# Performance work log

Measured on AMD Instinct MI355X. Metric: run time of the kernel, lower is better.

The kernel has to match this reference:

```python
import jax, jax.numpy as jnp
import numpy as np

D_MODEL = 1024
NUM_HEADS = 16
D_K = D_MODEL // NUM_HEADS


def setup_inputs() -> dict:
    key = jax.random.key(0)
    ks = jax.random.split(key, 12)
    B, S = 1, 4096
    s = 1.0 / np.sqrt(D_MODEL)
    inp = {
        'query': jax.random.normal(ks[0], (B, S, D_MODEL), jnp.float32),
        'key': jax.random.normal(ks[1], (B, S, D_MODEL), jnp.float32),
        'value': jax.random.normal(ks[2], (B, S, D_MODEL), jnp.float32),
        'W_q': jax.random.normal(ks[3], (D_MODEL, D_MODEL), jnp.float32) * s,
        'b_q': jnp.zeros((D_MODEL,), jnp.float32),
        'W_k': jax.random.normal(ks[4], (D_MODEL, D_MODEL), jnp.float32) * s,
        'b_k': jnp.zeros((D_MODEL,), jnp.float32),
        'W_v': jax.random.normal(ks[5], (D_MODEL, D_MODEL), jnp.float32) * s,
        'b_v': jnp.zeros((D_MODEL,), jnp.float32),
        'W_o': jax.random.normal(ks[6], (D_MODEL, D_MODEL), jnp.float32) * s,
        'b_o': jnp.zeros((D_MODEL,), jnp.float32),
    }
    return inp


def reference(query, key, value, W_q, b_q, W_k, b_k, W_v, b_v, W_o, b_o):
    B, S, _ = query.shape
    # torch nn.Linear: y = x @ W.T + b
    Q = query @ W_q.T + b_q
    K = key @ W_k.T + b_k
    V = value @ W_v.T + b_v
    # (B, S, H, d_k) -> (B, H, S, d_k)
    Q = Q.reshape(B, S, NUM_HEADS, D_K).transpose(0, 2, 1, 3)
    K = K.reshape(B, S, NUM_HEADS, D_K).transpose(0, 2, 1, 3)
    V = V.reshape(B, S, NUM_HEADS, D_K).transpose(0, 2, 1, 3)
    scale = 1.0 / jnp.sqrt(jnp.asarray(D_K, Q.dtype))
    qk = jnp.einsum('bhqd,bhkd->bhqk', Q, K) * scale  # [B,H,S,S]
    attn = jax.nn.softmax(qk, axis=-1)
    out = jnp.einsum('bhqk,bhkd->bhqd', attn, V)
    out = out.transpose(0, 2, 1, 3).reshape(B, S, D_MODEL)
    return out @ W_o.T + b_o
```

## Files before the change

kernel.cpp:

```cpp
#include <hip/hip_runtime.h>
#include <cstdint>
#include <cstddef>

typedef __bf16 bf16_t;
typedef _Float16 f16_t;
typedef __attribute__((ext_vector_type(8))) __bf16 bf16x8;
typedef __attribute__((ext_vector_type(4))) __bf16 bf16x4;
typedef __attribute__((ext_vector_type(2))) __bf16 bf16x2;
typedef __attribute__((ext_vector_type(8))) _Float16 f16x8;
typedef __attribute__((ext_vector_type(2))) _Float16 f16x2;
typedef __attribute__((ext_vector_type(4))) float floatx4;
typedef __attribute__((ext_vector_type(16))) float floatx16;

#define S_LEN 4096
#define DM 1024
#define NH 16
#define DKH 64
#define NSPLIT 4
#define KT_PER (S_LEN / 64 / NSPLIT)

#define QSCALE 0.1803368801111601f

__device__ __forceinline__ void async_b128(void* lds, const void* g) {
    __builtin_amdgcn_global_load_lds(
        (__attribute__((address_space(1))) void*)(uintptr_t)g,
        (__attribute__((address_space(3))) void*)lds,
        16, 0, 0);
}

__device__ __forceinline__ floatx4 mfma16(bf16x8 a, bf16x8 b, floatx4 c) {
    return __builtin_amdgcn_mfma_f32_16x16x32_bf16(a, b, c, 0, 0, 0);
}
__device__ __forceinline__ floatx16 mfma32(bf16x8 a, bf16x8 b, floatx16 c) {
    return __builtin_amdgcn_mfma_f32_32x32x16_bf16(a, b, c, 0, 0, 0);
}
__device__ __forceinline__ int f2i(float x) { return __builtin_bit_cast(int, x); }
__device__ __forceinline__ float i2f(int x) { return __builtin_bit_cast(float, x); }
__device__ __forceinline__ int p2i(bf16x2 x) { return __builtin_bit_cast(int, x); }
__device__ __forceinline__ bf16x2 i2p(int x) { return __builtin_bit_cast(bf16x2, x); }

__global__ __launch_bounds__(256) void convert_in_kernel(
    const float* __restrict__ q, const float* __restrict__ k,
    const float* __restrict__ v, bf16_t* __restrict__ dst) {
    const int z = blockIdx.z;
    const float* s = (z == 0) ? q : (z == 1) ? k : v;
    bf16_t* d = dst + (size_t)z * (S_LEN * DM);
    const size_t i = ((size_t)blockIdx.x * 256 + threadIdx.x) * 4;
    const floatx4 val = *(const floatx4*)(s + i);
    bf16x4 o;
    o[0] = (bf16_t)val[0]; o[1] = (bf16_t)val[1];
    o[2] = (bf16_t)val[2]; o[3] = (bf16_t)val[3];
    *(bf16x4*)(d + i) = o;
}

__global__ __launch_bounds__(256) void convert_w_kernel(
    const float* __restrict__ a, const float* __restrict__ b,
    const float* __restrict__ c, const float* __restrict__ e,
    bf16_t* __restrict__ dst) {
    const int z = blockIdx.z;
    const float* s = (z == 0) ? a : (z == 1) ? b : (z == 2) ? c : e;
    bf16_t* d = dst + (size_t)z * (DM * DM);
    const size_t i = ((size_t)blockIdx.x * 256 + threadIdx.x) * 4;
    const floatx4 val = *(const floatx4*)(s + i);
    bf16x4 o;
    o[0] = (bf16_t)val[0]; o[1] = (bf16_t)val[1];
    o[2] = (bf16_t)val[2]; o[3] = (bf16_t)val[3];
    *(bf16x4*)(d + i) = o;
}

template <int BN, typename OutT>
__device__ __forceinline__ void gemm_bt_body(const bf16_t* __restrict__ A,
                                             const bf16_t* __restrict__ B,
                                             const float* __restrict__ bias,
                                             OutT* __restrict__ C, float oscale) {
    constexpr int K = 1024, N = 1024;
    constexpr int NT = BN / 32;
    __shared__ bf16_t As[128 * 32];
    __shared__ bf16_t Bs[BN * 32];
    const int tid = threadIdx.x;
    const int wid = tid >> 6, lane = tid & 63;
    const int quad = lane >> 4, l16 = lane & 15;
    const int m0 = blockIdx.y * 128, n0 = blockIdx.x * BN;
    const int wm = (wid & 1) * 64, wn = (wid >> 1) * (BN / 2);

    floatx4 acc[4][NT] = {};

    for (int k0 = 0; k0 < K; k0 += 32) {
        __syncthreads();
#pragma unroll
        for (int i = 0; i < 2; ++i) {
            const int c = (i << 8) + tid;
            const int row = c >> 2;
            const int ko = (c & 3) << 3;
            const int lb = ((i << 8) + (wid << 6)) << 3;
            async_b128(&As[lb], A + (size_t)(m0 + row) * K + k0 + ko);
        }
#pragma unroll
        for (int i = 0; i < BN / 64; ++i) {
            const int c = (i << 8) + tid;
            const int row = c >> 2;
            const int ko = (c & 3) << 3;
            const int lb = ((i << 8) + (wid << 6)) << 3;
            async_b128(&Bs[lb], B + (size_t)(n0 + row) * K + k0 + ko);
        }
        __syncthreads();

        bf16x8 af[4], bfr[NT];
#pragma unroll
        for (int t = 0; t < 4; ++t)
            af[t] = *(const bf16x8*)&As[(wm + t * 16 + l16) * 32 + quad * 8];
#pragma unroll
        for (int t = 0; t < NT; ++t)
            bfr[t] = *(const bf16x8*)&Bs[(wn + t * 16 + l16) * 32 + quad * 8];
#pragma unroll
        for (int mt = 0; mt < 4; ++mt)
#pragma unroll
            for (int nt = 0; nt < NT; ++nt)
                acc[mt][nt] = mfma16(af[mt], bfr[nt], acc[mt][nt]);
    }

#pragma unroll
    for (int mt = 0; mt < 4; ++mt)
#pragma unroll
        for (int nt = 0; nt < NT; ++nt) {
            const int col = n0 + wn + nt * 16 + l16;
            const float bv = bias[col];
#pragma unroll
            for (int r = 0; r < 4; ++r) {
                const int row = m0 + wm + mt * 16 + quad * 4 + r;
                C[(size_t)row * N + col] = (OutT)((acc[mt][nt][r] + bv) * oscale);
            }
        }
}

__global__ __launch_bounds__(256) void gemm_qkv_kernel(
    const bf16_t* __restrict__ qx, const bf16_t* __restrict__ kx,
    const bf16_t* __restrict__ vx, const bf16_t* __restrict__ wq,
    const bf16_t* __restrict__ wk, const bf16_t* __restrict__ wv,
    const float* __restrict__ bq, const float* __restrict__ bk,
    const float* __restrict__ bv, bf16_t* __restrict__ Qp,
    bf16_t* __restrict__ Kp, bf16_t* __restrict__ Vp) {
    const int z = blockIdx.z;
    const bf16_t* A = (z == 0) ? qx : (z == 1) ? kx : vx;
    const bf16_t* B = (z == 0) ? wq : (z == 1) ? wk : wv;
    const float* bias = (z == 0) ? bq : (z == 1) ? bk : bv;
    bf16_t* C = (z == 0) ? Qp : (z == 1) ? Kp : Vp;
    gemm_bt_body<128, bf16_t>(A, B, bias, C, (z == 0) ? QSCALE : 1.0f);
}

__global__ __launch_bounds__(256) void gemm_out_kernel(
    const bf16_t* __restrict__ AO, const bf16_t* __restrict__ wo,
    const float* __restrict__ bo, float* __restrict__ out) {
    gemm_bt_body<64, float>(AO, wo, bo, out, 1.0f);
}

__global__ __launch_bounds__(256) void transpose_kernel(
    const bf16_t* __restrict__ in, bf16_t* __restrict__ out) {
    __shared__ bf16_t tile[64][65];
    const int tx = threadIdx.x & 63;
    const int ty = threadIdx.x >> 6;
    const int c0 = blockIdx.x * 64;
    const int r0 = blockIdx.y * 64;
#pragma unroll
    for (int i = 0; i < 16; ++i) {
        const int r = ty + i * 4;
        tile[r][tx] = in[(size_t)(r0 + r) * DM + c0 + tx];
    }
    __syncthreads();
#pragma unroll
    for (int i = 0; i < 16; ++i) {
        const int c = ty + i * 4;
        out[(size_t)(c0 + c) * S_LEN + r0 + tx] = tile[tx][c];
    }
}

__global__ __launch_bounds__(128, 2) void flash_kernel(
    const bf16_t* __restrict__ Q, const bf16_t* __restrict__ K,
    const bf16_t* __restrict__ Vt, f16_t* __restrict__ Opart,
    float* __restrict__ Lpart) {
    __shared__ bf16_t smem[16384];
    bf16_t* Ks = smem;
    bf16_t* Vs = smem + 8192;

    const int tid = threadIdx.x;
    const int wave = tid >> 6, lane = tid & 63;
    const int h32 = lane >> 5, c = lane & 31;
    const int head = blockIdx.y;
    const int sp = blockIdx.z;
    const int qbase = blockIdx.x * 128 + wave * 64;
    const int kv0 = sp * (S_LEN / NSPLIT);

    bf16x8 Qf[2][4];
#pragma unroll
    for (int nt = 0; nt < 2; ++nt)
#pragma unroll
        for (int s = 0; s < 4; ++s)
            Qf[nt][s] = *(const bf16x8*)(Q + (size_t)(qbase + nt * 32 + c) * DM +
                                         head * DKH + s * 16 + h32 * 8);

    floatx16 oa[2][2] = {};
    floatx4 la[2] = {};

    const bf16_t* kptr = K + (size_t)(kv0 + lane) * DM + head * DKH + wave * 32;
    const bf16_t* vptr = Vt + (size_t)(head * DKH + lane) * S_LEN + kv0 + wave * 32;
    bf16_t* ksl = Ks + wave * 2048;
    bf16_t* vsl = Vs + wave * 2048;

#pragma unroll
    for (int i = 0; i < 4; ++i) {
        async_b128(ksl + i * 512, kptr + i * 8);
        async_b128(vsl + i * 512, vptr + i * 8);
    }
    kptr += 64 * DM; vptr += 64;

    for (int kt = 0; kt < KT_PER; ++kt) {
        const int buf = kt & 1;
        __syncthreads();
        if (kt + 1 < KT_PER) {
#pragma unroll
            for (int i = 0; i < 4; ++i) {
                async_b128(ksl + (buf ^ 1) * 4096 + i * 512, kptr + i * 8);
                async_b128(vsl + (buf ^ 1) * 4096 + i * 512, vptr + i * 8);
            }
            kptr += 64 * DM; vptr += 64;
        }

        bf16x8 Kf[2][4];
#pragma unroll
        for (int mt = 0; mt < 2; ++mt)
#pragma unroll
            for (int s = 0; s < 4; ++s)
                Kf[mt][s] = *(const bf16x8*)&Ks[buf * 4096 + ((2 * s + h32) * 64 + mt * 32 + c) * 8];

        floatx16 sc[2][2] = {};
#pragma unroll
        for (int s = 0; s < 4; ++s)
#pragma unroll
            for (int mt = 0; mt < 2; ++mt)
#pragma unroll
                for (int nt = 0; nt < 2; ++nt)
                    sc[mt][nt] = mfma32(Kf[mt][s], Qf[nt][s], sc[mt][nt]);

        bf16x8 Vf[2][4];
#pragma unroll
        for (int dt = 0; dt < 2; ++dt)
#pragma unroll
            for (int s = 0; s < 4; ++s)
                Vf[dt][s] = *(const bf16x8*)&Vs[buf * 4096 + ((2 * s + h32) * 64 + dt * 32 + c) * 8];

#pragma unroll
        for (int nt = 0; nt < 2; ++nt) {
            bf16x2 pk[2][8];
#pragma unroll
            for (int mt = 0; mt < 2; ++mt)
#pragma unroll
                for (int rr = 0; rr < 8; ++rr) {
                    const float p0 = __builtin_amdgcn_exp2f(sc[mt][nt][2 * rr] - 3.0f);
                    const float p1 = __builtin_amdgcn_exp2f(sc[mt][nt][2 * rr + 1] - 3.0f);
                    la[nt][(2 * rr) & 3] += p0;
                    la[nt][(2 * rr + 1) & 3] += p1;
                    bf16x2 w; w[0] = (bf16_t)p0; w[1] = (bf16_t)p1;
                    pk[mt][rr] = w;
                }
#pragma unroll
            for (int s = 0; s < 4; ++s) {
                const int a = s >> 1, b4 = (s & 1) * 4;
                const bf16x2 r0 = h32 ? pk[a][b4 + 2] : pk[a][b4 + 0];
                const bf16x2 r1 = h32 ? pk[a][b4 + 3] : pk[a][b4 + 1];
                const bf16x2 s0 = h32 ? pk[a][b4 + 0] : pk[a][b4 + 2];
                const bf16x2 s1 = h32 ? pk[a][b4 + 1] : pk[a][b4 + 3];
                const bf16x2 x0 = i2p(__shfl_xor(p2i(s0), 32));
                const bf16x2 x1 = i2p(__shfl_xor(p2i(s1), 32));
                union { bf16x8 v; bf16x2 d[4]; } P;
                P.d[0] = h32 ? x0 : r0;
                P.d[1] = h32 ? x1 : r1;
                P.d[2] = h32 ? r0 : x0;
                P.d[3] = h32 ? r1 : x1;
                oa[0][nt] = mfma32(Vf[0][s], P.v, oa[0][nt]);
                oa[1][nt] = mfma32(Vf[1][s], P.v, oa[1][nt]);
            }
        }
    }

#pragma unroll
    for (int nt = 0; nt < 2; ++nt) {
        float t = la[nt][0] + la[nt][1] + la[nt][2] + la[nt][3];
        t += i2f(__shfl_xor(f2i(t), 32));
        if (h32 == 0)
            Lpart[(size_t)(sp * NH + head) * S_LEN + qbase + nt * 32 + c] = t;
    }

    __syncthreads();
    f16_t* ot = (f16_t*)smem + wave * (32 * 72);
#pragma unroll
    for (int nt = 0; nt < 2; ++nt) {
#pragma unroll
        for (int dt = 0; dt < 2; ++dt)
#pragma unroll
            for (int rr = 0; rr < 8; ++rr) {
                const int d0 = dt * 32 + ((2 * rr) & 3) + 8 * (rr >> 1) + 4 * h32;
                f16x2 w;
                w[0] = (f16_t)oa[dt][nt][2 * rr];
                w[1] = (f16_t)oa[dt][nt][2 * rr + 1];
                *(f16x2*)&ot[c * 72 + d0] = w;
            }
        __syncthreads();
        const int r = lane & 31;
#pragma unroll
        for (int j = 0; j < 4; ++j) {
            const f16x8 v = *(const f16x8*)&ot[r * 72 + h32 * 32 + j * 8];
            *(f16x8*)(Opart + ((size_t)sp * S_LEN + qbase + nt * 32 + r) * DM +
                      head * DKH + h32 * 32 + j * 8) = v;
        }
    }
}

__global__ __launch_bounds__(256) void reduce_kernel(
    const f16_t* __restrict__ Op, const float* __restrict__ Lp,
    bf16_t* __restrict__ AO) {
    const size_t f = ((size_t)blockIdx.x * 256 + threadIdx.x) * 8;
    const int q = (int)(f >> 10);
    const int h = (int)((f & 1023) >> 6);
    float l = 0.f;
#pragma unroll
    for (int sp = 0; sp < NSPLIT; ++sp)
        l += Lp[(size_t)(sp * NH + h) * S_LEN + q];
    const float inv = 1.0f / l;
    float s[8] = {};
#pragma unroll
    for (int sp = 0; sp < NSPLIT; ++sp) {
        const f16x8 v = *(const f16x8*)(Op + (size_t)sp * (S_LEN * DM) + f);
#pragma unroll
        for (int j = 0; j < 8; ++j) s[j] += (float)v[j];
    }
    bf16x8 o;
#pragma unroll
    for (int j = 0; j < 8; ++j) o[j] = (bf16_t)(s[j] * inv);
    *(bf16x8*)(AO + f) = o;
}

extern "C" void kernel_launch(void* const* d_in, const int* in_sizes, int n_in,
                              void* d_out, int out_size, void* d_ws, size_t ws_size,
                              hipStream_t stream) {
    const float* q  = (const float*)d_in[0];
    const float* k  = (const float*)d_in[1];
    const float* v  = (const float*)d_in[2];
    const float* Wq = (const float*)d_in[3];
    const float* bq = (const float*)d_in[4];
    const float* Wk = (const float*)d_in[5];
    const float* bk = (const float*)d_in[6];
    const float* Wv = (const float*)d_in[7];
    const float* bv = (const float*)d_in[8];
    const float* Wo = (const float*)d_in[9];
    const float* bo = (const float*)d_in[10];
    float* out = (float*)d_out;

    bf16_t* ws = (bf16_t*)d_ws;
    bf16_t* qx = ws;
    bf16_t* kx = qx + 4194304;
    bf16_t* vx = kx + 4194304;
    bf16_t* Vp = vx + 4194304;
    f16_t*  Opart = (f16_t*)ws;
    bf16_t* wq = Vp + 4194304;
    bf16_t* wk = wq + 1048576;
    bf16_t* wv = wk + 1048576;
    bf16_t* wo = wv + 1048576;
    bf16_t* Qp = wo + 1048576;
    bf16_t* Kp = Qp + 4194304;
    bf16_t* Vt = Kp + 4194304;
    bf16_t* AO = Vt + 4194304;
    float*  Lpart = (float*)(AO + 4194304);

    convert_in_kernel<<<dim3(4096, 1, 3), 256, 0, stream>>>(q, k, v, qx);
    convert_w_kernel<<<dim3(1024, 1, 4), 256, 0, stream>>>(Wq, Wk, Wv, Wo, wq);
    gemm_qkv_kernel<<<dim3(8, 32, 3), 256, 0, stream>>>(qx, kx, vx, wq, wk, wv,
                                                        bq, bk, bv, Qp, Kp, Vp);
    transpose_kernel<<<dim3(16, 64), 256, 0, stream>>>(Vp, Vt);
    flash_kernel<<<dim3(32, 16, NSPLIT), 128, 0, stream>>>(Qp, Kp, Vt, Opart, Lpart);
    reduce_kernel<<<dim3(2048), 256, 0, stream>>>(Opart, Lpart, AO);
    gemm_out_kernel<<<dim3(16, 32), 256, 0, stream>>>(AO, wo, bo, out);
    (void)in_sizes; (void)n_in; (void)out_size; (void)ws_size;
}
```

Before: 297.5 us.

## Merge conversion kernels and widen flash blocks to four waves sharing K/V tiles

```diff
diff --git a/kernel.cpp b/kernel.cpp
--- a/kernel.cpp
+++ b/kernel.cpp
@@ -39,33 +39,33 @@
 __device__ __forceinline__ int p2i(bf16x2 x) { return __builtin_bit_cast(int, x); }
 __device__ __forceinline__ bf16x2 i2p(int x) { return __builtin_bit_cast(bf16x2, x); }
 
-__global__ __launch_bounds__(256) void convert_in_kernel(
+__global__ __launch_bounds__(256) void convert_all_kernel(
     const float* __restrict__ q, const float* __restrict__ k,
-    const float* __restrict__ v, bf16_t* __restrict__ dst) {
-    const int z = blockIdx.z;
-    const float* s = (z == 0) ? q : (z == 1) ? k : v;
-    bf16_t* d = dst + (size_t)z * (S_LEN * DM);
+    const float* __restrict__ v, const float* __restrict__ wqf,
+    const float* __restrict__ wkf, const float* __restrict__ wvf,
+    const float* __restrict__ wof, bf16_t* __restrict__ dst_in,
+    bf16_t* __restrict__ dst_w) {
     const size_t i = ((size_t)blockIdx.x * 256 + threadIdx.x) * 4;
-    const floatx4 val = *(const floatx4*)(s + i);
+    const float* s;
+    bf16_t* d;
+    size_t off;
+    if (i < 12582912) {
+        const int r = (int)(i >> 22);
+        s = (r == 0) ? q : (r == 1) ? k : v;
+        off = i & 4194303;
+        d = dst_in + (size_t)r * 4194304 + off;
+    } else {
+        const size_t j = i - 12582912;
+        const int r = (int)(j >> 20);
+        s = (r == 0) ? wqf : (r == 1) ? wkf : (r == 2) ? wvf : wof;
+        off = j & 1048575;
+        d = dst_w + (size_t)r * 1048576 + off;
+    }
+    const floatx4 val = *(const floatx4*)(s + off);
     bf16x4 o;
     o[0] = (bf16_t)val[0]; o[1] = (bf16_t)val[1];
     o[2] = (bf16_t)val[2]; o[3] = (bf16_t)val[3];
-    *(bf16x4*)(d + i) = o;
-}
-
-__global__ __launch_bounds__(256) void convert_w_kernel(
-    const float* __restrict__ a, const float* __restrict__ b,
-    const float* __restrict__ c, const float* __restrict__ e,
-    bf16_t* __restrict__ dst) {
-    const int z = blockIdx.z;
-    const float* s = (z == 0) ? a : (z == 1) ? b : (z == 2) ? c : e;
-    bf16_t* d = dst + (size_t)z * (DM * DM);
-    const size_t i = ((size_t)blockIdx.x * 256 + threadIdx.x) * 4;
-    const floatx4 val = *(const floatx4*)(s + i);
-    bf16x4 o;
-    o[0] = (bf16_t)val[0]; o[1] = (bf16_t)val[1];
-    o[2] = (bf16_t)val[2]; o[3] = (bf16_t)val[3];
-    *(bf16x4*)(d + i) = o;
+    *(bf16x4*)d = o;
 }
 
 template <int BN, typename OutT>
@@ -174,7 +174,7 @@
     }
 }
 
-__global__ __launch_bounds__(128, 2) void flash_kernel(
+__global__ __launch_bounds__(256, 4) void flash_kernel(
     const bf16_t* __restrict__ Q, const bf16_t* __restrict__ K,
     const bf16_t* __restrict__ Vt, f16_t* __restrict__ Opart,
     float* __restrict__ Lpart) {
@@ -187,7 +187,7 @@
     const int h32 = lane >> 5, c = lane & 31;
     const int head = blockIdx.y;
     const int sp = blockIdx.z;
-    const int qbase = blockIdx.x * 128 + wave * 64;
+    const int qbase = blockIdx.x * 256 + wave * 64;
     const int kv0 = sp * (S_LEN / NSPLIT);
 
     bf16x8 Qf[2][4];
@@ -201,27 +201,23 @@
     floatx16 oa[2][2] = {};
     floatx4 la[2] = {};
 
-    const bf16_t* kptr = K + (size_t)(kv0 + lane) * DM + head * DKH + wave * 32;
-    const bf16_t* vptr = Vt + (size_t)(head * DKH + lane) * S_LEN + kv0 + wave * 32;
-    bf16_t* ksl = Ks + wave * 2048;
-    bf16_t* vsl = Vs + wave * 2048;
-
-#pragma unroll
-    for (int i = 0; i < 4; ++i) {
-        async_b128(ksl + i * 512, kptr + i * 8);
-        async_b128(vsl + i * 512, vptr + i * 8);
-    }
+    const bf16_t* kptr = K + (size_t)(kv0 + lane) * DM + head * DKH + wave * 16;
+    const bf16_t* vptr = Vt + (size_t)(head * DKH + lane) * S_LEN + kv0 + wave * 16;
+    bf16_t* ksl = Ks + wave * 1024;
+    bf16_t* vsl = Vs + wave * 1024;
+
+    async_b128(ksl, kptr);       async_b128(ksl + 512, kptr + 8);
+    async_b128(vsl, vptr);       async_b128(vsl + 512, vptr + 8);
     kptr += 64 * DM; vptr += 64;
 
     for (int kt = 0; kt < KT_PER; ++kt) {
         const int buf = kt & 1;
         __syncthreads();
         if (kt + 1 < KT_PER) {
-#pragma unroll
-            for (int i = 0; i < 4; ++i) {
-                async_b128(ksl + (buf ^ 1) * 4096 + i * 512, kptr + i * 8);
-                async_b128(vsl + (buf ^ 1) * 4096 + i * 512, vptr + i * 8);
-            }
+            bf16_t* kd = ksl + (buf ^ 1) * 4096;
+            bf16_t* vd = vsl + (buf ^ 1) * 4096;
+            async_b128(kd, kptr);     async_b128(kd + 512, kptr + 8);
+            async_b128(vd, vptr);     async_b128(vd + 512, vptr + 8);
             kptr += 64 * DM; vptr += 64;
         }
 
@@ -371,12 +367,12 @@
     bf16_t* AO = Vt + 4194304;
     float*  Lpart = (float*)(AO + 4194304);
 
-    convert_in_kernel<<<dim3(4096, 1, 3), 256, 0, stream>>>(q, k, v, qx);
-    convert_w_kernel<<<dim3(1024, 1, 4), 256, 0, stream>>>(Wq, Wk, Wv, Wo, wq);
+    convert_all_kernel<<<dim3(16384), 256, 0, stream>>>(q, k, v, Wq, Wk, Wv, Wo,
+                                                        qx, wq);
     gemm_qkv_kernel<<<dim3(8, 32, 3), 256, 0, stream>>>(qx, kx, vx, wq, wk, wv,
                                                         bq, bk, bv, Qp, Kp, Vp);
     transpose_kernel<<<dim3(16, 64), 256, 0, stream>>>(Vp, Vt);
-    flash_kernel<<<dim3(32, 16, NSPLIT), 128, 0, stream>>>(Qp, Kp, Vt, Opart, Lpart);
+    flash_kernel<<<dim3(16, 16, NSPLIT), 256, 0, stream>>>(Qp, Kp, Vt, Opart, Lpart);
     reduce_kernel<<<dim3(2048), 256, 0, stream>>>(Opart, Lpart, AO);
     gemm_out_kernel<<<dim3(16, 32), 256, 0, stream>>>(AO, wo, bo, out);
     (void)in_sizes; (void)n_in; (void)out_size; (void)ws_size;
```

Result: slower. 719.7 us (+141.9%).
